# Optimization experiments

Hardware: AMD Instinct MI355X
Metric: run time of the kernel (lower is better)

Reference implementation:

```python
import jax, jax.numpy as jnp
import numpy as np
import math

B, T, C = 4, 2048, 1024
H, DQK, DV = 16, 64, 64

def setup_inputs() -> dict:
    key = jax.random.key(0)
    k1, k2, k3, k4, k5 = jax.random.split(key, 5)
    # randw(*d) = randn(*d) / sqrt(d[-1])
    x_q = jax.random.normal(k1, (B, T, C), dtype=jnp.float32)
    w_q = jax.random.normal(k2, (H, DQK, C), dtype=jnp.float32) / math.sqrt(C)
    w_k = jax.random.normal(k3, (H, DQK, C), dtype=jnp.float32) / math.sqrt(C)
    w_v = jax.random.normal(k4, (H, DV, C), dtype=jnp.float32) / math.sqrt(C)
    w_o = jax.random.normal(k5, (DV * H, C), dtype=jnp.float32) / math.sqrt(C)
    return {"x_q": x_q, "w_q": w_q, "w_k": w_k, "w_v": w_v, "w_o": w_o}

def reference(x_q, w_q, w_k, w_v, w_o):
    # self-attention: x_kv = x_q
    q = jnp.einsum('ntc,hdc->nhtd', x_q, w_q)
    k = jnp.einsum('ntc,hdc->nhtd', x_q, w_k)
    v = jnp.einsum('ntc,hdc->nhtd', x_q, w_v)
    a = jnp.einsum('nhtd,nhsd->nhts', q, k) / math.sqrt(q.shape[3])
    t = a.shape[2]
    causal_forbidden = jnp.arange(t)[:, None] < jnp.arange(t)[None, :]  # [T,S]
    a = jnp.where(causal_forbidden[None, None], -jnp.inf, a)
    a = jax.nn.softmax(a, axis=3)
    y = jnp.einsum('nhts,nhsd->nthd', a, v).reshape(a.shape[0], t, -1)
    return y @ w_o
```

## Files before the change

### kernel.cpp

```cpp
#include <hip/hip_runtime.h>
#include <stdint.h>

#define B_ 4
#define T_ 2048
#define C_ 1024
#define H_ 16
#define D_ 64
#define M_ (B_*T_)
#define K_ C_

typedef unsigned short ushort_t;
typedef __bf16 bf16x8 __attribute__((ext_vector_type(8)));
typedef float  float4_ __attribute__((ext_vector_type(4)));
typedef ushort_t ushort4_ __attribute__((ext_vector_type(4)));
typedef uint32_t uint32x2 __attribute__((ext_vector_type(2)));

__device__ __forceinline__ ushort_t f2bf(float f) {
    union { float f; uint32_t u; } c; c.f = f;
    uint32_t u = c.u;
    uint32_t r = (u + 0x7FFFu + ((u >> 16) & 1u)) >> 16;
    return (ushort_t)r;
}
__device__ __forceinline__ float4_ f4zero() { float4_ z; z[0]=0.f; z[1]=0.f; z[2]=0.f; z[3]=0.f; return z; }

__device__ __forceinline__ uint32_t cvtpk(float a, float b) {
    uint32_t r;
    asm("v_cvt_pk_bf16_f32 %0, %1, %2" : "=v"(r) : "v"(a), "v"(b));
    return r;
}

#define GLDS16(gptr, lptr) \
    __builtin_amdgcn_global_load_lds((const __attribute__((address_space(1))) uint32_t*)(gptr), \
                                     (__attribute__((address_space(3))) uint32_t*)(lptr), 16, 0, 0)

__global__ __launch_bounds__(256) void cvt_f32_bf16(const float* __restrict__ src,
                                                    ushort_t* __restrict__ dst) {
    const int i = (blockIdx.x * 256 + threadIdx.x) * 4;
    float4_ v = *(const float4_*)(src + i);
    ushort4_ o;
    #pragma unroll
    for (int e = 0; e < 4; e++) o[e] = f2bf(v[e]);
    *(ushort4_*)(dst + i) = o;
}

__global__ __launch_bounds__(256) void cvt3_f32_bf16(const float* __restrict__ s0,
                                                     const float* __restrict__ s1,
                                                     const float* __restrict__ s2,
                                                     ushort_t* __restrict__ dst) {
    const int b = blockIdx.x;
    const float* src = (b < 1024) ? s0 : (b < 2048) ? s1 : s2;
    const int off = (b & 1023) * 1024 + threadIdx.x * 4;
    float4_ v = *(const float4_*)(src + off);
    ushort4_ o;
    #pragma unroll
    for (int e = 0; e < 4; e++) o[e] = f2bf(v[e]);
    *(ushort4_*)(dst + (size_t)b * 1024 + threadIdx.x * 4) = o;
}

__global__ __launch_bounds__(256) void transpose_wo(const float* __restrict__ wo,
                                                    ushort_t* __restrict__ wot) {
    __shared__ ushort_t tile[64][65];
    const int c0 = (blockIdx.x & 15) * 64;
    const int r0 = (blockIdx.x >> 4) * 64;
    const int tid = threadIdx.x;
    const int row = tid >> 2;
    const int col = (tid & 3) * 16;
    #pragma unroll
    for (int r = 0; r < 4; r++) {
        float4_ v = *(const float4_*)(wo + (size_t)(r0 + row) * 1024 + c0 + col + r * 4);
        #pragma unroll
        for (int e = 0; e < 4; e++) tile[row][col + r * 4 + e] = f2bf(v[e]);
    }
    __syncthreads();
    #pragma unroll
    for (int r = 0; r < 2; r++) {
        bf16x8 v;
        #pragma unroll
        for (int e = 0; e < 8; e++) v[e] = __builtin_bit_cast(__bf16, tile[col + r * 8 + e][row]);
        *(bf16x8*)(wot + (size_t)(c0 + row) * 1024 + r0 + col + r * 8) = v;
    }
}

template<int MODE>
__global__ __launch_bounds__(256)
void gemm_bt(const ushort_t* __restrict__ A,
             const ushort_t* __restrict__ Bt,
             ushort_t* __restrict__ q_ws, ushort_t* __restrict__ k_ws,
             ushort_t* __restrict__ vt_ws, float* __restrict__ outp)
{
    __shared__ __align__(16) ushort_t As[128 * 32];
    __shared__ __align__(16) ushort_t Bs[128 * 32];
    const int tid = threadIdx.x;
    const int m0 = blockIdx.x * 128;
    const int n0 = blockIdx.y * 128;

    const int L    = tid & 63;
    const int wid  = tid >> 6;
    const int wr   = (wid >> 1) * 64;
    const int wc   = (wid & 1) * 64;
    const int quad = L >> 4;
    const int lc   = L & 15;

    float4_ acc[4][4];
    #pragma unroll
    for (int i = 0; i < 4; i++)
        #pragma unroll
        for (int j = 0; j < 4; j++) acc[i][j] = f4zero();

    const int loff0 = wid * 1024 + L * 16;
    for (int k0 = 0; k0 < K_; k0 += 32) {
        __syncthreads();
        #pragma unroll
        for (int r = 0; r < 2; r++) {
            const int off = loff0 + r * 4096;
            const int row = off >> 6;
            const int col = off & 63;
            const char* ga = (const char*)A  + (size_t)(m0 + row) * (K_ * 2) + k0 * 2 + col;
            const char* gb = (const char*)Bt + (size_t)(n0 + row) * (K_ * 2) + k0 * 2 + col;
            GLDS16(ga, (char*)As + off);
            GLDS16(gb, (char*)Bs + off);
        }
        __syncthreads();
        bf16x8 af[4], bfr[4];
        #pragma unroll
        for (int i = 0; i < 4; i++) {
            const int m = wr + i * 16 + lc;
            af[i]  = *(const bf16x8*)((const char*)As + m * 64 + quad * 16);
            const int n = wc + i * 16 + lc;
            bfr[i] = *(const bf16x8*)((const char*)Bs + n * 64 + quad * 16);
        }
        #pragma unroll
        for (int i = 0; i < 4; i++)
            #pragma unroll
            for (int j = 0; j < 4; j++)
                acc[i][j] = __builtin_amdgcn_mfma_f32_16x16x32_bf16(af[i], bfr[j], acc[i][j], 0, 0, 0);
    }

    const int mat = n0 >> 10;
    const int nb  = n0 & 1023;
    #pragma unroll
    for (int i = 0; i < 4; i++) {
        #pragma unroll
        for (int j = 0; j < 4; j++) {
            #pragma unroll
            for (int rg = 0; rg < 4; rg++) {
                const int mg = m0 + wr + i * 16 + quad * 4 + rg;
                const float v = acc[i][j][rg];
                if (MODE == 1) {
                    const int cg = n0 + wc + j * 16 + lc;
                    outp[(size_t)mg * 1024 + cg] = v;
                } else {
                    const int ln = nb + wc + j * 16 + lc;
                    const int h = ln >> 6, d = ln & 63;
                    const int n = mg >> 11, t = mg & 2047;
                    const int nh = n * H_ + h;
                    if (mat == 0)      q_ws [((size_t)nh * T_ + t) * 64 + d] = f2bf(v * 0.18033688011112042f);
                    else if (mat == 1) k_ws [((size_t)nh * T_ + t) * 64 + d] = f2bf(v);
                    else               vt_ws[((size_t)nh * 64 + d) * T_ + t] = f2bf(v);
                }
            }
        }
    }
}

#define KP 72

__global__ __launch_bounds__(512)
void attn(const ushort_t* __restrict__ q_ws, const ushort_t* __restrict__ k_ws,
          const ushort_t* __restrict__ vt_ws, ushort_t* __restrict__ y_ws)
{
    __shared__ __align__(16) ushort_t Ks[2][64 * 64];
    __shared__ __align__(16) ushort_t Vs[2][64 * 64];
    __shared__ __align__(16) ushort_t Ps[8][16 * KP];
    const int tid  = threadIdx.x;
    const int L    = tid & 63;
    const int w    = tid >> 6;
    const int quad = L >> 4, lc = L & 15;
    const int bid  = blockIdx.x;
    const int qt   = 15 - (bid >> 6);
    const int nh   = bid & 63;
    const int n    = nh >> 4;
    const int tq0  = qt * 128 + w * 16;
    const int tg   = tq0 + lc;
    const int nt   = 2 * qt + 2;
    const int dstile = tq0 >> 6;

    const ushort_t* qbase = q_ws + ((size_t)nh * T_ + tq0) * 64;
    const bf16x8 qf0 = *(const bf16x8*)(qbase + (size_t)lc * 64 + quad * 8);
    const bf16x8 qf1 = *(const bf16x8*)(qbase + (size_t)lc * 64 + quad * 8 + 32);

    float m_i = -1e30f, l_i = 0.f;
    float4_ o[4];
    #pragma unroll
    for (int r = 0; r < 4; r++) o[r] = f4zero();

    const char* kbase = (const char*)(k_ws  + (size_t)nh * T_ * 64);
    const char* vbase = (const char*)(vt_ws + (size_t)nh * 64 * T_);
    char* pwr = (char*)Ps[w] + lc * (KP * 2);

    const int ldsoff = tid * 16;
    const int srow   = ldsoff >> 7;
    const int sslot  = (ldsoff >> 4) & 7;
    const int sgs    = sslot ^ (srow & 7);
    const size_t kgo = (size_t)srow * 128 + sgs * 16;
    const size_t vgo = (size_t)srow * (T_ * 2) + sgs * 16;

    int off16[4][2];
    #pragma unroll
    for (int b = 0; b < 4; b++) {
        const int row = b * 16 + lc;
        const int r7  = lc & 7;
        off16[b][0] = row * 128 + ((quad ^ r7) << 4);
        off16[b][1] = row * 128 + (((quad + 4) ^ r7) << 4);
    }

    auto STAGE = [&](int st, int b) {
        GLDS16(kbase + (size_t)st * 8192 + kgo, (char*)Ks[b] + ldsoff);
        GLDS16(vbase + (size_t)st * 128  + vgo, (char*)Vs[b] + ldsoff);
    };

    STAGE(0, 0);
    __syncthreads();
    int cur = 0;

    for (int st = 0; st < nt; st++) {
        if (st + 1 < nt) STAGE(st + 1, cur ^ 1);
        if (st * 64 <= tq0 + 15) {
            const char* ks = (const char*)Ks[cur];
            const char* vs = (const char*)Vs[cur];

            float4_ s[4];
            #pragma unroll
            for (int sb = 0; sb < 4; sb++) {
                const bf16x8 kf0 = *(const bf16x8*)(ks + off16[sb][0]);
                const bf16x8 kf1 = *(const bf16x8*)(ks + off16[sb][1]);
                float4_ a = f4zero();
                a = __builtin_amdgcn_mfma_f32_16x16x32_bf16(kf0, qf0, a, 0, 0, 0);
                a = __builtin_amdgcn_mfma_f32_16x16x32_bf16(kf1, qf1, a, 0, 0, 0);
                s[sb] = a;
            }
            if (st >= dstile) {
                #pragma unroll
                for (int sb = 0; sb < 4; sb++)
                    #pragma unroll
                    for (int rg = 0; rg < 4; rg++) {
                        const int sg = st * 64 + sb * 16 + quad * 4 + rg;
                        if (sg > tg) s[sb][rg] = -1e30f;
                    }
            }
            float rm = -1e30f;
            #pragma unroll
            for (int sb = 0; sb < 4; sb++)
                #pragma unroll
                for (int rg = 0; rg < 4; rg++) rm = fmaxf(rm, s[sb][rg]);
            rm = fmaxf(rm, __shfl_xor(rm, 16));
            rm = fmaxf(rm, __shfl_xor(rm, 32));
            if (!__all(rm <= m_i + 8.f)) {
                const float mn    = fmaxf(m_i, rm);
                const float alpha = __builtin_amdgcn_exp2f(m_i - mn);
                l_i *= alpha;
                #pragma unroll
                for (int db = 0; db < 4; db++)
                    #pragma unroll
                    for (int rg = 0; rg < 4; rg++) o[db][rg] *= alpha;
                m_i = mn;
            }
            float rs = 0.f;
            #pragma unroll
            for (int sb = 0; sb < 4; sb++)
                #pragma unroll
                for (int rg = 0; rg < 4; rg++) {
                    const float p = __builtin_amdgcn_exp2f(s[sb][rg] - m_i);
                    s[sb][rg] = p;
                    rs += p;
                }
            rs += __shfl_xor(rs, 16);
            rs += __shfl_xor(rs, 32);
            l_i += rs;

            #pragma unroll
            for (int sb = 0; sb < 4; sb++) {
                uint32x2 pk2;
                pk2[0] = cvtpk(s[sb][0], s[sb][1]);
                pk2[1] = cvtpk(s[sb][2], s[sb][3]);
                *(uint32x2*)(pwr + sb * 32 + quad * 8) = pk2;
            }

            const bf16x8 pa0 = *(const bf16x8*)(pwr + quad * 16);
            const bf16x8 pa1 = *(const bf16x8*)(pwr + 64 + quad * 16);
            #pragma unroll
            for (int db = 0; db < 4; db++) {
                const bf16x8 vf0 = *(const bf16x8*)(vs + off16[db][0]);
                const bf16x8 vf1 = *(const bf16x8*)(vs + off16[db][1]);
                o[db] = __builtin_amdgcn_mfma_f32_16x16x32_bf16(vf0, pa0, o[db], 0, 0, 0);
                o[db] = __builtin_amdgcn_mfma_f32_16x16x32_bf16(vf1, pa1, o[db], 0, 0, 0);
            }
        }
        __syncthreads();
        cur ^= 1;
    }

    const int h = nh & 15;
    const float inv = 1.f / l_i;
    ushort_t* yrow = y_ws + ((size_t)(n * T_ + tg)) * 1024 + h * 64;
    #pragma unroll
    for (int db = 0; db < 4; db++) {
        uint32x2 pk2;
        pk2[0] = cvtpk(o[db][0] * inv, o[db][1] * inv);
        pk2[1] = cvtpk(o[db][2] * inv, o[db][3] * inv);
        *(uint32x2*)(yrow + db * 16 + quad * 4) = pk2;
    }
}

extern "C" void kernel_launch(void* const* d_in, const int* in_sizes, int n_in,
                              void* d_out, int out_size, void* d_ws, size_t ws_size,
                              hipStream_t stream) {
    (void)in_sizes; (void)n_in; (void)out_size; (void)ws_size;
    const float* x  = (const float*)d_in[0];
    const float* wq = (const float*)d_in[1];
    const float* wk = (const float*)d_in[2];
    const float* wv = (const float*)d_in[3];
    const float* wo = (const float*)d_in[4];
    char* ws = (char*)d_ws;
    const size_t MB = (size_t)1024 * 1024;
    ushort_t* x_bf  = (ushort_t*)(ws);
    ushort_t* q_ws  = (ushort_t*)(ws + 16 * MB);
    ushort_t* k_ws  = (ushort_t*)(ws + 32 * MB);
    ushort_t* vt_ws = (ushort_t*)(ws + 48 * MB);
    ushort_t* wcat  = (ushort_t*)(ws + 64 * MB);
    ushort_t* wot   = (ushort_t*)(ws + 70 * MB);
    ushort_t* y_ws  = x_bf;
    float*    outp  = (float*)d_out;

    cvt_f32_bf16<<<dim3(8192), dim3(256), 0, stream>>>(x, x_bf);
    cvt3_f32_bf16<<<dim3(3072), dim3(256), 0, stream>>>(wq, wk, wv, wcat);
    transpose_wo<<<dim3(256), dim3(256), 0, stream>>>(wo, wot);
    gemm_bt<0><<<dim3(64, 24), dim3(256), 0, stream>>>(x_bf, wcat, q_ws, k_ws, vt_ws, nullptr);
    attn<<<dim3(1024), dim3(512), 0, stream>>>(q_ws, k_ws, vt_ws, y_ws);
    gemm_bt<1><<<dim3(64, 8), dim3(256), 0, stream>>>(y_ws, wot, nullptr, nullptr, nullptr, outp);
}
```

Baseline: 258.0 us.

## Replace GEMM with 8-wave 256x128 tile, double-buffered swizzled LDS pipeline

Replaces the 4-wave 128x128 GEMM, which had two barriers per K=32 step, with a 512-thread kernel on 256x128 tiles and K=64 steps. Global-to-LDS loads are double-buffered and issued ahead of the MFMA phases, with explicit vmcnt waits and raw s_barrier calls. LDS rows are XOR-swizzled to avoid bank conflicts, and MFMA phases run at raised priority. The goal is to hide load latency and cut sync overhead in the QKV and output projections. In exchange it uses more LDS and registers, and the hand-scheduled barrier and waitcnt sequence is fragile.

```diff
diff --git a/kernel.cpp b/kernel.cpp
--- a/kernel.cpp
+++ b/kernel.cpp
@@ -32,6 +32,9 @@
 #define GLDS16(gptr, lptr) \
     __builtin_amdgcn_global_load_lds((const __attribute__((address_space(1))) uint32_t*)(gptr), \
                                      (__attribute__((address_space(3))) uint32_t*)(lptr), 16, 0, 0)
+
+#define BARRIER() asm volatile("s_barrier" ::: "memory")
+#define VMCNT(n)  asm volatile("s_waitcnt vmcnt(" #n ")" ::: "memory")
 
 __global__ __launch_bounds__(256) void cvt_f32_bf16(const float* __restrict__ src,
                                                     ushort_t* __restrict__ dst) {
@@ -82,24 +85,63 @@
 }
 
 template<int MODE>
-__global__ __launch_bounds__(256)
-void gemm_bt(const ushort_t* __restrict__ A,
-             const ushort_t* __restrict__ Bt,
-             ushort_t* __restrict__ q_ws, ushort_t* __restrict__ k_ws,
-             ushort_t* __restrict__ vt_ws, float* __restrict__ outp)
+__global__ __launch_bounds__(512, 2)
+void gemm8(const ushort_t* __restrict__ A,
+           const ushort_t* __restrict__ Bt,
+           ushort_t* __restrict__ q_ws, ushort_t* __restrict__ k_ws,
+           ushort_t* __restrict__ vt_ws, float* __restrict__ outp)
 {
-    __shared__ __align__(16) ushort_t As[128 * 32];
-    __shared__ __align__(16) ushort_t Bs[128 * 32];
+    __shared__ __align__(16) ushort_t As8[2][2][128 * 64];
+    __shared__ __align__(16) ushort_t Bs8[2][128 * 64];
     const int tid = threadIdx.x;
-    const int m0 = blockIdx.x * 128;
+    const int m0 = blockIdx.x * 256;
     const int n0 = blockIdx.y * 128;
-
-    const int L    = tid & 63;
-    const int wid  = tid >> 6;
-    const int wr   = (wid >> 1) * 64;
-    const int wc   = (wid & 1) * 64;
-    const int quad = L >> 4;
-    const int lc   = L & 15;
+    const int L = tid & 63, wid = tid >> 6;
+    const int wm = wid >> 1;
+    const int wn = wid & 1;
+    const int quad = L >> 4, lc = L & 15;
+
+    size_t a_src[2], b_src[2];
+    int    l_off[2];
+    #pragma unroll
+    for (int q = 0; q < 2; q++) {
+        const int off = tid * 16 + q * 8192;
+        const int lr = off >> 7, slot = (off >> 4) & 7;
+        const int sp = slot ^ (lr & 7);
+        l_off[q] = off;
+        a_src[q] = (size_t)(m0 + (lr >> 5) * 64 + (lr & 31)) * 2048 + sp * 16;
+        b_src[q] = (size_t)(n0 + lr) * 2048 + sp * 16;
+    }
+    const char* Ag = (const char*)A;
+    const char* Bg = (const char*)Bt;
+
+    auto STAGE_A = [&](int c, int h, int kt) {
+        #pragma unroll
+        for (int q = 0; q < 2; q++)
+            GLDS16(Ag + a_src[q] + (size_t)h * 65536 + (size_t)kt * 128,
+                   (char*)As8[c][h] + l_off[q]);
+    };
+    auto STAGE_B = [&](int c, int kt) {
+        #pragma unroll
+        for (int q = 0; q < 2; q++)
+            GLDS16(Bg + b_src[q] + (size_t)kt * 128, (char*)Bs8[c] + l_off[q]);
+    };
+
+    int offA[2][2], offB[4][2];
+    #pragma unroll
+    for (int mi2 = 0; mi2 < 2; mi2++)
+        #pragma unroll
+        for (int ks = 0; ks < 2; ks++) {
+            const int lr = wm * 32 + mi2 * 16 + lc;
+            offA[mi2][ks] = lr * 128 + (((ks * 4 + quad) ^ (lc & 7)) << 4);
+        }
+    #pragma unroll
+    for (int nj = 0; nj < 4; nj++)
+        #pragma unroll
+        for (int ks = 0; ks < 2; ks++) {
+            const int row = wn * 64 + nj * 16 + lc;
+            offB[nj][ks] = row * 128 + (((ks * 4 + quad) ^ (lc & 7)) << 4);
+        }
 
     float4_ acc[4][4];
     #pragma unroll
@@ -107,37 +149,91 @@
         #pragma unroll
         for (int j = 0; j < 4; j++) acc[i][j] = f4zero();
 
-    const int loff0 = wid * 1024 + L * 16;
-    for (int k0 = 0; k0 < K_; k0 += 32) {
-        __syncthreads();
-        #pragma unroll
-        for (int r = 0; r < 2; r++) {
-            const int off = loff0 + r * 4096;
-            const int row = off >> 6;
-            const int col = off & 63;
-            const char* ga = (const char*)A  + (size_t)(m0 + row) * (K_ * 2) + k0 * 2 + col;
-            const char* gb = (const char*)Bt + (size_t)(n0 + row) * (K_ * 2) + k0 * 2 + col;
-            GLDS16(ga, (char*)As + off);
-            GLDS16(gb, (char*)Bs + off);
-        }
-        __syncthreads();
-        bf16x8 af[4], bfr[4];
-        #pragma unroll
-        for (int i = 0; i < 4; i++) {
-            const int m = wr + i * 16 + lc;
-            af[i]  = *(const bf16x8*)((const char*)As + m * 64 + quad * 16);
-            const int n = wc + i * 16 + lc;
-            bfr[i] = *(const bf16x8*)((const char*)Bs + n * 64 + quad * 16);
-        }
-        #pragma unroll
-        for (int i = 0; i < 4; i++)
-            #pragma unroll
-            for (int j = 0; j < 4; j++)
-                acc[i][j] = __builtin_amdgcn_mfma_f32_16x16x32_bf16(af[i], bfr[j], acc[i][j], 0, 0, 0);
-    }
+#define LOAD_AF(AF, c, h) \
+    _Pragma("unroll") for (int mi2_ = 0; mi2_ < 2; mi2_++) \
+    _Pragma("unroll") for (int ks_ = 0; ks_ < 2; ks_++) \
+        AF[mi2_][ks_] = *(const bf16x8*)((const char*)As8[c][h] + offA[mi2_][ks_]);
+#define LOAD_BF(c) \
+    _Pragma("unroll") for (int nj_ = 0; nj_ < 4; nj_++) \
+    _Pragma("unroll") for (int ks_ = 0; ks_ < 2; ks_++) \
+        bfr[nj_][ks_] = *(const bf16x8*)((const char*)Bs8[c] + offB[nj_][ks_]);
+#define PHASE_MFMA(AF, MB) \
+    __builtin_amdgcn_s_setprio(1); \
+    _Pragma("unroll") for (int mi2_ = 0; mi2_ < 2; mi2_++) \
+    _Pragma("unroll") for (int nj_ = 0; nj_ < 4; nj_++) { \
+        acc[(MB) + mi2_][nj_] = __builtin_amdgcn_mfma_f32_16x16x32_bf16(AF[mi2_][0], bfr[nj_][0], acc[(MB) + mi2_][nj_], 0, 0, 0); \
+        acc[(MB) + mi2_][nj_] = __builtin_amdgcn_mfma_f32_16x16x32_bf16(AF[mi2_][1], bfr[nj_][1], acc[(MB) + mi2_][nj_], 0, 0, 0); \
+    } \
+    __builtin_amdgcn_s_setprio(0);
+
+    STAGE_A(0, 0, 0);
+    STAGE_A(0, 1, 0);
+    STAGE_B(0, 0);
+    STAGE_A(1, 0, 1);
+    VMCNT(2);
+    BARRIER();
+
+    bf16x8 bfr[4][2];
+    bf16x8 af0[2][2], af1[2][2];
+
+    for (int i = 0; i < 7; i++) {
+        const int kt1 = 2 * i + 1;
+        LOAD_AF(af0, 0, 0);
+        LOAD_BF(0);
+        STAGE_A(1, 1, kt1);
+        BARRIER();
+        PHASE_MFMA(af0, 0);
+        BARRIER();
+        LOAD_AF(af1, 0, 1);
+        STAGE_B(1, kt1);
+        STAGE_A(0, 0, kt1 + 1);
+        BARRIER();
+        PHASE_MFMA(af1, 2);
+        VMCNT(2);
+        BARRIER();
+        LOAD_AF(af0, 1, 0);
+        LOAD_BF(1);
+        STAGE_A(0, 1, kt1 + 1);
+        BARRIER();
+        PHASE_MFMA(af0, 0);
+        BARRIER();
+        LOAD_AF(af1, 1, 1);
+        STAGE_B(0, kt1 + 1);
+        STAGE_A(1, 0, kt1 + 2);
+        BARRIER();
+        PHASE_MFMA(af1, 2);
+        VMCNT(2);
+        BARRIER();
+    }
+    LOAD_AF(af0, 0, 0);
+    LOAD_BF(0);
+    STAGE_A(1, 1, 15);
+    BARRIER();
+    PHASE_MFMA(af0, 0);
+    BARRIER();
+    LOAD_AF(af1, 0, 1);
+    STAGE_B(1, 15);
+    BARRIER();
+    PHASE_MFMA(af1, 2);
+    VMCNT(0);
+    BARRIER();
+    LOAD_AF(af0, 1, 0);
+    LOAD_BF(1);
+    BARRIER();
+    PHASE_MFMA(af0, 0);
+    BARRIER();
+    LOAD_AF(af1, 1, 1);
+    BARRIER();
+    PHASE_MFMA(af1, 2);
+
+#undef LOAD_AF
+#undef LOAD_BF
+#undef PHASE_MFMA
 
     const int mat = n0 >> 10;
     const int nb  = n0 & 1023;
+    const int wr  = wm * 64;
+    const int wc  = wn * 64;
     #pragma unroll
     for (int i = 0; i < 4; i++) {
         #pragma unroll
@@ -335,7 +431,7 @@
     cvt_f32_bf16<<<dim3(8192), dim3(256), 0, stream>>>(x, x_bf);
     cvt3_f32_bf16<<<dim3(3072), dim3(256), 0, stream>>>(wq, wk, wv, wcat);
     transpose_wo<<<dim3(256), dim3(256), 0, stream>>>(wo, wot);
-    gemm_bt<0><<<dim3(64, 24), dim3(256), 0, stream>>>(x_bf, wcat, q_ws, k_ws, vt_ws, nullptr);
+    gemm8<0><<<dim3(32, 24), dim3(512), 0, stream>>>(x_bf, wcat, q_ws, k_ws, vt_ws, nullptr);
     attn<<<dim3(1024), dim3(512), 0, stream>>>(q_ws, k_ws, vt_ws, y_ws);
-    gemm_bt<1><<<dim3(64, 8), dim3(256), 0, stream>>>(y_ws, wot, nullptr, nullptr, nullptr, outp);
-}
+    gemm8<1><<<dim3(32, 8), dim3(512), 0, stream>>>(y_ws, wot, nullptr, nullptr, nullptr, outp);
+}
```

Measured after the change: 259.0 us. No clear change (+0.4%).

## Replace GEMMs with 8-wave 256x128 triple-buffered swizzled LDS pipeline

Applied to the files above, without the earlier changes.

Rewrites the projection GEMM kernel to use 512-thread blocks covering 256x128 output tiles with a K-step of 64. Tiles live in triple-buffered shared memory filled by direct global-to-LDS loads issued two tiles ahead, with XOR-swizzled addressing to avoid bank conflicts. The old kernel had a full sync around every 32-wide K step, so loads were never overlapped with MFMA work; the new scheme interleaves loads with compute using manual barriers, vmcnt waits and setprio. It uses about 144KB of LDS per block and launches half as many blocks, which may hurt occupancy and the tail on the smaller output GEMM.

```diff
diff --git a/kernel.cpp b/kernel.cpp
--- a/kernel.cpp
+++ b/kernel.cpp
@@ -32,6 +32,9 @@
 #define GLDS16(gptr, lptr) \
     __builtin_amdgcn_global_load_lds((const __attribute__((address_space(1))) uint32_t*)(gptr), \
                                      (__attribute__((address_space(3))) uint32_t*)(lptr), 16, 0, 0)
+
+#define BARRIER() asm volatile("s_barrier" ::: "memory")
+#define VMCNT(n)  asm volatile("s_waitcnt vmcnt(" #n ")" ::: "memory")
 
 __global__ __launch_bounds__(256) void cvt_f32_bf16(const float* __restrict__ src,
                                                     ushort_t* __restrict__ dst) {
@@ -82,24 +85,53 @@
 }
 
 template<int MODE>
-__global__ __launch_bounds__(256)
-void gemm_bt(const ushort_t* __restrict__ A,
-             const ushort_t* __restrict__ Bt,
-             ushort_t* __restrict__ q_ws, ushort_t* __restrict__ k_ws,
-             ushort_t* __restrict__ vt_ws, float* __restrict__ outp)
+__global__ __launch_bounds__(512, 2)
+void gemm8(const ushort_t* __restrict__ A,
+           const ushort_t* __restrict__ Bt,
+           ushort_t* __restrict__ q_ws, ushort_t* __restrict__ k_ws,
+           ushort_t* __restrict__ vt_ws, float* __restrict__ outp)
 {
-    __shared__ __align__(16) ushort_t As[128 * 32];
-    __shared__ __align__(16) ushort_t Bs[128 * 32];
+    __shared__ __align__(16) ushort_t As3[3][256 * 64];
+    __shared__ __align__(16) ushort_t Bs3[3][128 * 64];
     const int tid = threadIdx.x;
-    const int m0 = blockIdx.x * 128;
+    const int m0 = blockIdx.x * 256;
     const int n0 = blockIdx.y * 128;
-
-    const int L    = tid & 63;
-    const int wid  = tid >> 6;
-    const int wr   = (wid >> 1) * 64;
-    const int wc   = (wid & 1) * 64;
-    const int quad = L >> 4;
-    const int lc   = L & 15;
+    const int L = tid & 63, wid = tid >> 6;
+    const int wm = wid >> 1;
+    const int wn = wid & 1;
+    const int quad = L >> 4, lc = L & 15;
+
+    const int loff = tid * 16;
+    const int lr   = loff >> 7;
+    const int sp   = ((loff >> 4) & 7) ^ (lr & 7);
+    size_t a_src[4], b_src[2];
+    #pragma unroll
+    for (int q = 0; q < 4; q++)
+        a_src[q] = (size_t)(m0 + q * 64 + lr) * 2048 + sp * 16;
+    #pragma unroll
+    for (int q = 0; q < 2; q++)
+        b_src[q] = (size_t)(n0 + q * 64 + lr) * 2048 + sp * 16;
+    const char* Ag = (const char*)A;
+    const char* Bg = (const char*)Bt;
+
+#define SA(c, q, kt) GLDS16(Ag + a_src[q] + (size_t)(kt) * 128, (char*)As3[c] + (q) * 8192 + loff)
+#define SB(c, q, kt) GLDS16(Bg + b_src[q] + (size_t)(kt) * 128, (char*)Bs3[c] + (q) * 8192 + loff)
+
+    int offA[4][2], offB[4][2];
+    #pragma unroll
+    for (int mi = 0; mi < 4; mi++)
+        #pragma unroll
+        for (int ks = 0; ks < 2; ks++) {
+            const int row = wm * 64 + mi * 16 + lc;
+            offA[mi][ks] = row * 128 + (((ks * 4 + quad) ^ (lc & 7)) << 4);
+        }
+    #pragma unroll
+    for (int nj = 0; nj < 4; nj++)
+        #pragma unroll
+        for (int ks = 0; ks < 2; ks++) {
+            const int row = wn * 64 + nj * 16 + lc;
+            offB[nj][ks] = row * 128 + (((ks * 4 + quad) ^ (lc & 7)) << 4);
+        }
 
     float4_ acc[4][4];
     #pragma unroll
@@ -107,37 +139,67 @@
         #pragma unroll
         for (int j = 0; j < 4; j++) acc[i][j] = f4zero();
 
-    const int loff0 = wid * 1024 + L * 16;
-    for (int k0 = 0; k0 < K_; k0 += 32) {
-        __syncthreads();
-        #pragma unroll
-        for (int r = 0; r < 2; r++) {
-            const int off = loff0 + r * 4096;
-            const int row = off >> 6;
-            const int col = off & 63;
-            const char* ga = (const char*)A  + (size_t)(m0 + row) * (K_ * 2) + k0 * 2 + col;
-            const char* gb = (const char*)Bt + (size_t)(n0 + row) * (K_ * 2) + k0 * 2 + col;
-            GLDS16(ga, (char*)As + off);
-            GLDS16(gb, (char*)Bs + off);
-        }
-        __syncthreads();
-        bf16x8 af[4], bfr[4];
-        #pragma unroll
-        for (int i = 0; i < 4; i++) {
-            const int m = wr + i * 16 + lc;
-            af[i]  = *(const bf16x8*)((const char*)As + m * 64 + quad * 16);
-            const int n = wc + i * 16 + lc;
-            bfr[i] = *(const bf16x8*)((const char*)Bs + n * 64 + quad * 16);
-        }
-        #pragma unroll
-        for (int i = 0; i < 4; i++)
-            #pragma unroll
-            for (int j = 0; j < 4; j++)
-                acc[i][j] = __builtin_amdgcn_mfma_f32_16x16x32_bf16(af[i], bfr[j], acc[i][j], 0, 0, 0);
-    }
+    bf16x8 bfr[4][2];
+    bf16x8 af[2][2];
+
+#define LOAD_AF(c, mb) \
+    _Pragma("unroll") for (int mi2_ = 0; mi2_ < 2; mi2_++) \
+    _Pragma("unroll") for (int ks_ = 0; ks_ < 2; ks_++) \
+        af[mi2_][ks_] = *(const bf16x8*)((const char*)As3[c] + offA[(mb) + mi2_][ks_]);
+#define LOAD_BF(c) \
+    _Pragma("unroll") for (int nj_ = 0; nj_ < 4; nj_++) \
+    _Pragma("unroll") for (int ks_ = 0; ks_ < 2; ks_++) \
+        bfr[nj_][ks_] = *(const bf16x8*)((const char*)Bs3[c] + offB[nj_][ks_]);
+#define PHASE_MFMA(MB) \
+    __builtin_amdgcn_s_setprio(1); \
+    _Pragma("unroll") for (int mi2_ = 0; mi2_ < 2; mi2_++) \
+    _Pragma("unroll") for (int nj_ = 0; nj_ < 4; nj_++) { \
+        acc[(MB) + mi2_][nj_] = __builtin_amdgcn_mfma_f32_16x16x32_bf16(af[mi2_][0], bfr[nj_][0], acc[(MB) + mi2_][nj_], 0, 0, 0); \
+        acc[(MB) + mi2_][nj_] = __builtin_amdgcn_mfma_f32_16x16x32_bf16(af[mi2_][1], bfr[nj_][1], acc[(MB) + mi2_][nj_], 0, 0, 0); \
+    } \
+    __builtin_amdgcn_s_setprio(0);
+
+#define TILE(c, cn, t, DO_STAGE, GATE) \
+    LOAD_AF(c, 0); \
+    LOAD_BF(c); \
+    if (DO_STAGE) { SA(cn, 0, (t) + 2); SA(cn, 1, (t) + 2); SB(cn, 0, (t) + 2); } \
+    BARRIER(); \
+    PHASE_MFMA(0); \
+    BARRIER(); \
+    LOAD_AF(c, 2); \
+    if (DO_STAGE) { SA(cn, 2, (t) + 2); SA(cn, 3, (t) + 2); SB(cn, 1, (t) + 2); } \
+    BARRIER(); \
+    PHASE_MFMA(2); \
+    GATE; \
+    BARRIER();
+
+    SA(0, 0, 0); SA(0, 1, 0); SA(0, 2, 0); SA(0, 3, 0); SB(0, 0, 0); SB(0, 1, 0);
+    SA(1, 0, 1); SA(1, 1, 1); SA(1, 2, 1); SA(1, 3, 1); SB(1, 0, 1); SB(1, 1, 1);
+    VMCNT(6);
+    BARRIER();
+
+    for (int tb = 0; tb < 4; tb++) {
+        const int t0 = tb * 3;
+        TILE(0, 2, t0,     1, VMCNT(6));
+        TILE(1, 0, t0 + 1, 1, VMCNT(6));
+        TILE(2, 1, t0 + 2, 1, VMCNT(6));
+    }
+    TILE(0, 2, 12, 1, VMCNT(6));
+    TILE(1, 0, 13, 1, VMCNT(6));
+    TILE(2, 0, 14, 0, VMCNT(0));
+    TILE(0, 0, 15, 0, );
+
+#undef TILE
+#undef LOAD_AF
+#undef LOAD_BF
+#undef PHASE_MFMA
+#undef SA
+#undef SB
 
     const int mat = n0 >> 10;
     const int nb  = n0 & 1023;
+    const int wr  = wm * 64;
+    const int wc  = wn * 64;
     #pragma unroll
     for (int i = 0; i < 4; i++) {
         #pragma unroll
@@ -335,7 +397,7 @@
     cvt_f32_bf16<<<dim3(8192), dim3(256), 0, stream>>>(x, x_bf);
     cvt3_f32_bf16<<<dim3(3072), dim3(256), 0, stream>>>(wq, wk, wv, wcat);
     transpose_wo<<<dim3(256), dim3(256), 0, stream>>>(wo, wot);
-    gemm_bt<0><<<dim3(64, 24), dim3(256), 0, stream>>>(x_bf, wcat, q_ws, k_ws, vt_ws, nullptr);
+    gemm8<0><<<dim3(32, 24), dim3(512), 0, stream>>>(x_bf, wcat, q_ws, k_ws, vt_ws, nullptr);
     attn<<<dim3(1024), dim3(512), 0, stream>>>(q_ws, k_ws, vt_ws, y_ws);
-    gemm_bt<1><<<dim3(64, 8), dim3(256), 0, stream>>>(y_ws, wot, nullptr, nullptr, nullptr, outp);
-}
+    gemm8<1><<<dim3(32, 8), dim3(512), 0, stream>>>(y_ws, wot, nullptr, nullptr, nullptr, outp);
+}
```

Measured after the change: 254.3 us. About the same (-1.5%).
